# Kernel tuning notes

Measured on AMD Instinct MI355X. Metric: run time of the kernel, lower is better.

## Reference

```python
import jax, jax.numpy as jnp
import numpy as np

B, T, RNN_DIM, ENC_DIM, ATT_DIM, NFILT, KSIZE = 256, 1024, 1024, 512, 128, 32, 31
PAD = (KSIZE - 1) // 2


def setup_inputs() -> dict:
    key = jax.random.key(0)
    ks = jax.random.split(key, 10)
    attn = jax.random.uniform(ks[3], (B, T), dtype=jnp.float32)
    attn = attn / jnp.sum(attn, axis=1, keepdims=True)  # previous-step alignment (sums to 1)
    return {
        "query": jax.random.normal(ks[0], (B, RNN_DIM), dtype=jnp.float32),
        "memory": jax.random.normal(ks[1], (B, T, ENC_DIM), dtype=jnp.float32),
        "processed_memory": jax.random.normal(ks[2], (B, T, ATT_DIM), dtype=jnp.float32),
        "attn_weights": attn,
        "attn_weights_cum": jax.random.uniform(ks[4], (B, T), dtype=jnp.float32),
        "memory_lengths": jax.random.randint(ks[5], (B,), T // 2, T + 1),
        "conv_w": jax.random.normal(ks[6], (NFILT, 2, KSIZE), dtype=jnp.float32) * 0.1,
        "W_loc": jax.random.normal(ks[7], (ATT_DIM, NFILT), dtype=jnp.float32) * 0.1,
        "W_q": jax.random.normal(ks[8], (ATT_DIM, RNN_DIM), dtype=jnp.float32) * 0.03,
        "v_w": jax.random.normal(ks[9], (1, ATT_DIM), dtype=jnp.float32) * 0.1,
        "v_b": jnp.zeros((1,), dtype=jnp.float32),
    }


def reference(query, memory, processed_memory, attn_weights, attn_weights_cum,
              memory_lengths, conv_w, W_loc, W_q, v_w, v_b):
    Tlen = memory.shape[1]
    # [B, 2, T]: stack prev + cumulative alignments
    cat = jnp.stack([attn_weights, attn_weights_cum], axis=1)
    # location conv: Conv1d(2 -> NFILT, k=31, same padding, no bias) -> [B, NFILT, T]
    loc = jax.lax.conv_general_dilated(
        cat, conv_w, window_strides=(1,), padding=[(PAD, PAD)],
        dimension_numbers=("NCH", "OIH", "NCH"))
    # location_dense: [B, T, ATT_DIM]
    processed_location = jnp.einsum("bct,ac->bta", loc, W_loc)
    # query projection: [B, 1, ATT_DIM]
    processed_query = (query @ W_q.T)[:, None, :]
    # additive energies: v . tanh(q + loc + mem) -> [B, T]
    hidden = jnp.tanh(processed_query + processed_location + processed_memory)
    energies = jnp.einsum("bta,a->bt", hidden, v_w[0]) + v_b[0]
    # mask padded positions (pos >= length) with -inf
    mask = jnp.arange(Tlen)[None, :] >= memory_lengths[:, None]
    energies = jnp.where(mask, -jnp.inf, energies)
    new_attn = jax.nn.softmax(energies, axis=1)
    new_cum = attn_weights_cum + new_attn
    # context: [B, ENC_DIM]
    context = jnp.einsum("bt,bte->be", new_attn, memory)
    return context, new_attn, new_cum
```

## Files before the change

kernel.cpp:

```cpp
#include <hip/hip_runtime.h>
#include <math.h>

#define Bc 256
#define Tc 1024
#define RNN_DIMc 1024
#define ENC_DIMc 512
#define ATT_DIMc 128
#define NFILTc 32
#define KSIZEc 31
#define PADc 15

typedef float f4v __attribute__((ext_vector_type(4)));

__device__ __forceinline__ float fast_tanh(float x) {
    x = fminf(15.f, fmaxf(-15.f, x));
    float z = __expf(2.f * x);
    return (z - 1.f) / (z + 1.f);
}

__device__ __forceinline__ float wave_reduce_max(float x) {
#pragma unroll
    for (int off = 32; off > 0; off >>= 1) x = fmaxf(x, __shfl_xor(x, off, 64));
    return x;
}

__device__ __forceinline__ float wave_reduce_sum(float x) {
#pragma unroll
    for (int off = 32; off > 0; off >>= 1) x += __shfl_xor(x, off, 64);
    return x;
}

__global__ __launch_bounds__(1024) void lsa_fused(
    const float* __restrict__ query, const float* __restrict__ memory,
    const float* __restrict__ pm, const float* __restrict__ attn_w,
    const float* __restrict__ cum_w, const int* __restrict__ lens,
    const float* __restrict__ conv_w, const float* __restrict__ W_loc,
    const float* __restrict__ W_q, const float* __restrict__ v_w,
    const float* __restrict__ v_b, float* __restrict__ ctx,
    float* __restrict__ out_attn, float* __restrict__ out_cum) {
    const int b = blockIdx.x;
    const int tid = threadIdx.x;
    const int len = lens[b];

    __shared__ float s_q[RNN_DIMc];
    __shared__ float s_pq[ATT_DIMc];
    __shared__ float s_win0[Tc + 2 * PADc];
    __shared__ float s_win1[Tc + 2 * PADc];
    __shared__ float s_attn[Tc];
    __shared__ float s_redm[16];
    __shared__ float s_reds[16];
    __shared__ float s_ctx[16][ENC_DIMc];

    s_q[tid] = query[b * RNN_DIMc + tid];
    for (int i = tid; i < Tc + 2 * PADc; i += 1024) {
        int tt = i - PADc;
        bool ok = (tt >= 0) && (tt < Tc);
        s_win0[i] = ok ? attn_w[b * Tc + tt] : 0.f;
        s_win1[i] = ok ? cum_w[b * Tc + tt] : 0.f;
    }
    __syncthreads();

    {
        const int a = tid >> 3;
        const int c = tid & 7;
        const float* w = W_q + (size_t)a * RNN_DIMc;
        float acc = 0.f;
#pragma unroll 4
        for (int j = 0; j < 32; ++j) {
            const int r = c * 4 + j * 32;
            float4 wv = *(const float4*)(w + r);
            acc = fmaf(wv.x, s_q[r + 0], acc);
            acc = fmaf(wv.y, s_q[r + 1], acc);
            acc = fmaf(wv.z, s_q[r + 2], acc);
            acc = fmaf(wv.w, s_q[r + 3], acc);
        }
        acc += __shfl_xor(acc, 1, 64);
        acc += __shfl_xor(acc, 2, 64);
        acc += __shfl_xor(acc, 4, 64);
        if (c == 0) s_pq[a] = acc;
    }
    __syncthreads();

    const int t = tid;
    float e = -INFINITY;
    if (t < len) {
        float loc[NFILTc];
#pragma unroll
        for (int f = 0; f < NFILTc; ++f) loc[f] = 0.f;
        for (int k = 0; k < KSIZEc; ++k) {
            const float wa = s_win0[t + k];
            const float wc = s_win1[t + k];
#pragma unroll
            for (int f = 0; f < NFILTc; ++f) {
                loc[f] = fmaf(conv_w[f * (2 * KSIZEc) + k], wa, loc[f]);
                loc[f] = fmaf(conv_w[f * (2 * KSIZEc) + KSIZEc + k], wc, loc[f]);
            }
        }

        const float* pmrow = pm + ((size_t)(b * Tc + t)) * ATT_DIMc;
        float acc = 0.f;
#pragma unroll 2
        for (int a = 0; a < ATT_DIMc; a += 4) {
            const f4v pmv = __builtin_nontemporal_load((const f4v*)(pmrow + a));
            const float* wl = W_loc + a * NFILTc;
            float pl0 = 0.f, pl1 = 0.f, pl2 = 0.f, pl3 = 0.f;
#pragma unroll
            for (int f = 0; f < NFILTc; ++f) {
                float lf = loc[f];
                pl0 = fmaf(wl[f], lf, pl0);
                pl1 = fmaf(wl[NFILTc + f], lf, pl1);
                pl2 = fmaf(wl[2 * NFILTc + f], lf, pl2);
                pl3 = fmaf(wl[3 * NFILTc + f], lf, pl3);
            }
            acc = fmaf(v_w[a + 0], fast_tanh(s_pq[a + 0] + pl0 + pmv.x), acc);
            acc = fmaf(v_w[a + 1], fast_tanh(s_pq[a + 1] + pl1 + pmv.y), acc);
            acc = fmaf(v_w[a + 2], fast_tanh(s_pq[a + 2] + pl2 + pmv.z), acc);
            acc = fmaf(v_w[a + 3], fast_tanh(s_pq[a + 3] + pl3 + pmv.w), acc);
        }
        e = acc + v_b[0];
    }

    {
        float m = wave_reduce_max(e);
        if ((tid & 63) == 0) s_redm[tid >> 6] = m;
        __syncthreads();
        float bm = s_redm[0];
#pragma unroll
        for (int j = 1; j < 16; ++j) bm = fmaxf(bm, s_redm[j]);

        float p = __expf(e - bm);
        float s = wave_reduce_sum(p);
        if ((tid & 63) == 0) s_reds[tid >> 6] = s;
        __syncthreads();
        float tot = 0.f;
#pragma unroll
        for (int j = 0; j < 16; ++j) tot += s_reds[j];
        float na = p * (1.f / tot);

        out_attn[b * Tc + t] = na;
        out_cum[b * Tc + t] = s_win1[t + PADc] + na;
        s_attn[t] = na;
    }
    __syncthreads();

    {
        const int tr = tid >> 6;
        const int e8 = (tid & 63) * 8;
        const float* mb = memory + (size_t)b * Tc * ENC_DIMc;
        f4v acc0 = {0.f, 0.f, 0.f, 0.f};
        f4v acc1 = {0.f, 0.f, 0.f, 0.f};
#pragma unroll 4
        for (int tt = tr; tt < len; tt += 16) {
            const float w = s_attn[tt];
            const float* row = mb + (size_t)tt * ENC_DIMc + e8;
            const f4v m0 = __builtin_nontemporal_load((const f4v*)(row));
            const f4v m1 = __builtin_nontemporal_load((const f4v*)(row + 4));
            acc0.x = fmaf(w, m0.x, acc0.x);
            acc0.y = fmaf(w, m0.y, acc0.y);
            acc0.z = fmaf(w, m0.z, acc0.z);
            acc0.w = fmaf(w, m0.w, acc0.w);
            acc1.x = fmaf(w, m1.x, acc1.x);
            acc1.y = fmaf(w, m1.y, acc1.y);
            acc1.z = fmaf(w, m1.z, acc1.z);
            acc1.w = fmaf(w, m1.w, acc1.w);
        }
        *(f4v*)&s_ctx[tr][e8] = acc0;
        *(f4v*)&s_ctx[tr][e8 + 4] = acc1;
    }
    __syncthreads();
    if (tid < ENC_DIMc) {
        float s = 0.f;
#pragma unroll
        for (int j = 0; j < 16; ++j) s += s_ctx[j][tid];
        ctx[b * ENC_DIMc + tid] = s;
    }
}

extern "C" void kernel_launch(void* const* d_in, const int* in_sizes, int n_in,
                              void* d_out, int out_size, void* d_ws, size_t ws_size,
                              hipStream_t stream) {
    const float* query  = (const float*)d_in[0];
    const float* memory = (const float*)d_in[1];
    const float* pm     = (const float*)d_in[2];
    const float* attn_w = (const float*)d_in[3];
    const float* cum_w  = (const float*)d_in[4];
    const int*   lens   = (const int*)d_in[5];
    const float* conv_w = (const float*)d_in[6];
    const float* W_loc  = (const float*)d_in[7];
    const float* W_q    = (const float*)d_in[8];
    const float* v_w    = (const float*)d_in[9];
    const float* v_b    = (const float*)d_in[10];

    float* out      = (float*)d_out;
    float* ctx      = out;
    float* out_attn = out + Bc * ENC_DIMc;
    float* out_cum  = out + Bc * ENC_DIMc + Bc * Tc;


    lsa_fused<<<Bc, 1024, 0, stream>>>(query, memory, pm, attn_w, cum_w, lens,
                                       conv_w, W_loc, W_q, v_w, v_b,
                                       ctx, out_attn, out_cum);
}
```

Measured before the change: 799.3 us.

## Split context reduction into separate chunked kernels for more parallelism

The fused kernel becomes three launches. The first computes energies, softmax and the cumulative output. The second computes per-chunk partial context sums with 16 blocks per batch row. The third adds the partials into the final context. This spreads the memory read (the largest stream) over 4096 smaller blocks instead of 256 large ones, so HBM bandwidth use and occupancy should improve. The cost is two extra launches, writing and re-reading the attention weights and partials through global memory, and a workspace buffer.

```diff
diff --git a/kernel.cpp b/kernel.cpp
--- a/kernel.cpp
+++ b/kernel.cpp
@@ -9,6 +9,8 @@
 #define NFILTc 32
 #define KSIZEc 31
 #define PADc 15
+#define NCH 16
+#define CHT (Tc / NCH)
 
 typedef float f4v __attribute__((ext_vector_type(4)));
 
@@ -30,13 +32,12 @@
     return x;
 }
 
-__global__ __launch_bounds__(1024) void lsa_fused(
-    const float* __restrict__ query, const float* __restrict__ memory,
-    const float* __restrict__ pm, const float* __restrict__ attn_w,
-    const float* __restrict__ cum_w, const int* __restrict__ lens,
-    const float* __restrict__ conv_w, const float* __restrict__ W_loc,
-    const float* __restrict__ W_q, const float* __restrict__ v_w,
-    const float* __restrict__ v_b, float* __restrict__ ctx,
+__global__ __launch_bounds__(1024) void lsa_energy(
+    const float* __restrict__ query, const float* __restrict__ pm,
+    const float* __restrict__ attn_w, const float* __restrict__ cum_w,
+    const int* __restrict__ lens, const float* __restrict__ conv_w,
+    const float* __restrict__ W_loc, const float* __restrict__ W_q,
+    const float* __restrict__ v_w, const float* __restrict__ v_b,
     float* __restrict__ out_attn, float* __restrict__ out_cum) {
     const int b = blockIdx.x;
     const int tid = threadIdx.x;
@@ -46,10 +47,8 @@
     __shared__ float s_pq[ATT_DIMc];
     __shared__ float s_win0[Tc + 2 * PADc];
     __shared__ float s_win1[Tc + 2 * PADc];
-    __shared__ float s_attn[Tc];
     __shared__ float s_redm[16];
     __shared__ float s_reds[16];
-    __shared__ float s_ctx[16][ENC_DIMc];
 
     s_q[tid] = query[b * RNN_DIMc + tid];
     for (int i = tid; i < Tc + 2 * PADc; i += 1024) {
@@ -96,7 +95,6 @@
                 loc[f] = fmaf(conv_w[f * (2 * KSIZEc) + KSIZEc + k], wc, loc[f]);
             }
         }
-
         const float* pmrow = pm + ((size_t)(b * Tc + t)) * ATT_DIMc;
         float acc = 0.f;
 #pragma unroll 2
@@ -139,41 +137,66 @@
 
         out_attn[b * Tc + t] = na;
         out_cum[b * Tc + t] = s_win1[t + PADc] + na;
-        s_attn[t] = na;
-    }
-    __syncthreads();
-
-    {
-        const int tr = tid >> 6;
-        const int e8 = (tid & 63) * 8;
-        const float* mb = memory + (size_t)b * Tc * ENC_DIMc;
-        f4v acc0 = {0.f, 0.f, 0.f, 0.f};
-        f4v acc1 = {0.f, 0.f, 0.f, 0.f};
+    }
+}
+
+__global__ __launch_bounds__(256) void ctx_part_k(
+    const float* __restrict__ memory, const float* __restrict__ out_attn,
+    const int* __restrict__ lens, float* __restrict__ part) {
+    const int bc = blockIdx.x;
+    const int b = bc >> 4;
+    const int ch = bc & (NCH - 1);
+    const int t0 = ch * CHT;
+    const int tid = threadIdx.x;
+    const int len = lens[b];
+    if (t0 >= len) return;
+    int lim = len - t0;
+    if (lim > CHT) lim = CHT;
+
+    __shared__ float s_w[CHT];
+    __shared__ float s_part[4][ENC_DIMc];
+    if (tid < CHT) s_w[tid] = out_attn[b * Tc + t0 + tid];
+    __syncthreads();
+
+    const int tr = tid >> 6;
+    const int e8 = (tid & 63) * 8;
+    const float* mb = memory + ((size_t)(b * Tc + t0)) * ENC_DIMc;
+    f4v acc0 = {0.f, 0.f, 0.f, 0.f};
+    f4v acc1 = {0.f, 0.f, 0.f, 0.f};
 #pragma unroll 4
-        for (int tt = tr; tt < len; tt += 16) {
-            const float w = s_attn[tt];
-            const float* row = mb + (size_t)tt * ENC_DIMc + e8;
-            const f4v m0 = __builtin_nontemporal_load((const f4v*)(row));
-            const f4v m1 = __builtin_nontemporal_load((const f4v*)(row + 4));
-            acc0.x = fmaf(w, m0.x, acc0.x);
-            acc0.y = fmaf(w, m0.y, acc0.y);
-            acc0.z = fmaf(w, m0.z, acc0.z);
-            acc0.w = fmaf(w, m0.w, acc0.w);
-            acc1.x = fmaf(w, m1.x, acc1.x);
-            acc1.y = fmaf(w, m1.y, acc1.y);
-            acc1.z = fmaf(w, m1.z, acc1.z);
-            acc1.w = fmaf(w, m1.w, acc1.w);
-        }
-        *(f4v*)&s_ctx[tr][e8] = acc0;
-        *(f4v*)&s_ctx[tr][e8 + 4] = acc1;
-    }
-    __syncthreads();
-    if (tid < ENC_DIMc) {
-        float s = 0.f;
-#pragma unroll
-        for (int j = 0; j < 16; ++j) s += s_ctx[j][tid];
-        ctx[b * ENC_DIMc + tid] = s;
-    }
+    for (int tt = tr; tt < lim; tt += 4) {
+        const float w = s_w[tt];
+        const float* row = mb + (size_t)tt * ENC_DIMc + e8;
+        const f4v m0 = __builtin_nontemporal_load((const f4v*)(row));
+        const f4v m1 = __builtin_nontemporal_load((const f4v*)(row + 4));
+        acc0.x = fmaf(w, m0.x, acc0.x);
+        acc0.y = fmaf(w, m0.y, acc0.y);
+        acc0.z = fmaf(w, m0.z, acc0.z);
+        acc0.w = fmaf(w, m0.w, acc0.w);
+        acc1.x = fmaf(w, m1.x, acc1.x);
+        acc1.y = fmaf(w, m1.y, acc1.y);
+        acc1.z = fmaf(w, m1.z, acc1.z);
+        acc1.w = fmaf(w, m1.w, acc1.w);
+    }
+    *(f4v*)&s_part[tr][e8] = acc0;
+    *(f4v*)&s_part[tr][e8 + 4] = acc1;
+    __syncthreads();
+    for (int e2 = tid; e2 < ENC_DIMc; e2 += 256) {
+        float v = s_part[0][e2] + s_part[1][e2] + s_part[2][e2] + s_part[3][e2];
+        part[(size_t)bc * ENC_DIMc + e2] = v;
+    }
+}
+
+__global__ __launch_bounds__(512) void ctx_comb_k(
+    const float* __restrict__ part, const int* __restrict__ lens,
+    float* __restrict__ ctx) {
+    const int b = blockIdx.x;
+    const int tid = threadIdx.x;
+    const int nch = (lens[b] + CHT - 1) / CHT;
+    const float* p = part + (size_t)(b * NCH) * ENC_DIMc + tid;
+    float s = 0.f;
+    for (int ch = 0; ch < nch; ++ch) s += p[(size_t)ch * ENC_DIMc];
+    ctx[b * ENC_DIMc + tid] = s;
 }
 
 extern "C" void kernel_launch(void* const* d_in, const int* in_sizes, int n_in,
@@ -196,8 +219,11 @@
     float* out_attn = out + Bc * ENC_DIMc;
     float* out_cum  = out + Bc * ENC_DIMc + Bc * Tc;
 
-
-    lsa_fused<<<Bc, 1024, 0, stream>>>(query, memory, pm, attn_w, cum_w, lens,
-                                       conv_w, W_loc, W_q, v_w, v_b,
-                                       ctx, out_attn, out_cum);
-}
+    float* part = (float*)d_ws;
+
+    lsa_energy<<<Bc, 1024, 0, stream>>>(query, pm, attn_w, cum_w, lens,
+                                        conv_w, W_loc, W_q, v_w, v_b,
+                                        out_attn, out_cum);
+    ctx_part_k<<<Bc * NCH, 256, 0, stream>>>(memory, out_attn, lens, part);
+    ctx_comb_k<<<Bc, 512, 0, stream>>>(part, lens, ctx);
+}
```

After: 818.1 us. 1.02x slower.

## Convert fused attention kernel to persistent work queue with chunked context tasks

Applied to the files above, without the earlier changes.

Replaces the one-block-per-batch kernel with a persistent kernel of 1024 blocks of 256 threads. Blocks pull tasks from an atomic counter: first the per-batch energy and softmax tasks, then per-batch, per-time-chunk context partial sums. Context tasks wait on a release/acquire flag set when their batch's softmax finishes, and the last chunk to finish reduces the partials. The aim is to raise parallelism for the memory-bound context read over the 256 MB memory tensor, and to overlap it with energy work. This costs an extra init kernel, workspace traffic, spin-waiting and fewer threads per energy task.

```diff
diff --git a/kernel.cpp b/kernel.cpp
--- a/kernel.cpp
+++ b/kernel.cpp
@@ -9,6 +9,11 @@
 #define NFILTc 32
 #define KSIZEc 31
 #define PADc 15
+#define CHTc 128
+#define NCHc 8
+#define N_ENERGY Bc
+#define NTASKS (N_ENERGY + Bc * NCHc)
+#define FLAG_STRIDE 16
 
 typedef float f4v __attribute__((ext_vector_type(4)));
 
@@ -30,149 +35,212 @@
     return x;
 }
 
-__global__ __launch_bounds__(1024) void lsa_fused(
+__global__ __launch_bounds__(256) void init_k(int* __restrict__ ctrl) {
+    ctrl[blockIdx.x * 256 + threadIdx.x] = 0;
+}
+
+__global__ __launch_bounds__(256, 4) void lsa_persist(
     const float* __restrict__ query, const float* __restrict__ memory,
     const float* __restrict__ pm, const float* __restrict__ attn_w,
     const float* __restrict__ cum_w, const int* __restrict__ lens,
     const float* __restrict__ conv_w, const float* __restrict__ W_loc,
     const float* __restrict__ W_q, const float* __restrict__ v_w,
-    const float* __restrict__ v_b, float* __restrict__ ctx,
+    const float* __restrict__ v_b, int* __restrict__ ctrl,
+    float* __restrict__ part, float* __restrict__ ctx,
     float* __restrict__ out_attn, float* __restrict__ out_cum) {
-    const int b = blockIdx.x;
-    const int tid = threadIdx.x;
-    const int len = lens[b];
 
     __shared__ float s_q[RNN_DIMc];
     __shared__ float s_pq[ATT_DIMc];
+    __shared__ float s_pqh[ATT_DIMc];
     __shared__ float s_win0[Tc + 2 * PADc];
     __shared__ float s_win1[Tc + 2 * PADc];
-    __shared__ float s_attn[Tc];
-    __shared__ float s_redm[16];
-    __shared__ float s_reds[16];
-    __shared__ float s_ctx[16][ENC_DIMc];
-
-    s_q[tid] = query[b * RNN_DIMc + tid];
-    for (int i = tid; i < Tc + 2 * PADc; i += 1024) {
-        int tt = i - PADc;
-        bool ok = (tt >= 0) && (tt < Tc);
-        s_win0[i] = ok ? attn_w[b * Tc + tt] : 0.f;
-        s_win1[i] = ok ? cum_w[b * Tc + tt] : 0.f;
-    }
-    __syncthreads();
-
-    {
-        const int a = tid >> 3;
-        const int c = tid & 7;
-        const float* w = W_q + (size_t)a * RNN_DIMc;
-        float acc = 0.f;
+    __shared__ float s_e[Tc];
+    __shared__ float s_red[4];
+    __shared__ float s_red2[4];
+    __shared__ float s_w[CHTc];
+    __shared__ float s_part[4][ENC_DIMc];
+    __shared__ int s_task;
+    __shared__ int s_old;
+
+    const int tid = threadIdx.x;
+    int* flags   = ctrl;
+    int* done    = ctrl + Bc * FLAG_STRIDE;
+    int* counter = done + Bc;
+
+    while (true) {
+        __syncthreads();
+        if (tid == 0) s_task = atomicAdd(counter, 1);
+        __syncthreads();
+        const int task = s_task;
+        if (task >= NTASKS) return;
+
+        if (task < N_ENERGY) {
+            const int b = task;
+            const int len = lens[b];
+            {
+                const int i4 = tid * 4;
+                *(f4v*)&s_q[i4] = *(const f4v*)&query[(size_t)b * RNN_DIMc + i4];
+            }
+            for (int i = tid; i < Tc + 2 * PADc; i += 256) {
+                int tt = i - PADc;
+                bool ok = (tt >= 0) && (tt < Tc);
+                s_win0[i] = ok ? attn_w[b * Tc + tt] : 0.f;
+                s_win1[i] = ok ? cum_w[b * Tc + tt] : 0.f;
+            }
+            __syncthreads();
+            {
+                const int a = tid & 127;
+                const int h = tid >> 7;
+                const float* w = W_q + (size_t)a * RNN_DIMc + h * 512;
+                const float* qq = s_q + h * 512;
+                float acc = 0.f;
 #pragma unroll 4
-        for (int j = 0; j < 32; ++j) {
-            const int r = c * 4 + j * 32;
-            float4 wv = *(const float4*)(w + r);
-            acc = fmaf(wv.x, s_q[r + 0], acc);
-            acc = fmaf(wv.y, s_q[r + 1], acc);
-            acc = fmaf(wv.z, s_q[r + 2], acc);
-            acc = fmaf(wv.w, s_q[r + 3], acc);
+                for (int r = 0; r < 512; r += 4) {
+                    float4 wv = *(const float4*)(w + r);
+                    acc = fmaf(wv.x, qq[r + 0], acc);
+                    acc = fmaf(wv.y, qq[r + 1], acc);
+                    acc = fmaf(wv.z, qq[r + 2], acc);
+                    acc = fmaf(wv.w, qq[r + 3], acc);
+                }
+                if (h) s_pqh[a] = acc; else s_pq[a] = acc;
+            }
+            __syncthreads();
+            if (tid < ATT_DIMc) s_pq[tid] += s_pqh[tid];
+            __syncthreads();
+
+            for (int sct = 0; sct < 4; ++sct) {
+                const int t = (sct << 8) + tid;
+                float e = -INFINITY;
+                if (t < len) {
+                    float loc[NFILTc];
+#pragma unroll
+                    for (int f = 0; f < NFILTc; ++f) loc[f] = 0.f;
+                    for (int k = 0; k < KSIZEc; ++k) {
+                        const float wa = s_win0[t + k];
+                        const float wc = s_win1[t + k];
+#pragma unroll
+                        for (int f = 0; f < NFILTc; ++f) {
+                            loc[f] = fmaf(conv_w[f * (2 * KSIZEc) + k], wa, loc[f]);
+                            loc[f] = fmaf(conv_w[f * (2 * KSIZEc) + KSIZEc + k], wc, loc[f]);
+                        }
+                    }
+                    const float* pmrow = pm + ((size_t)(b * Tc + t)) * ATT_DIMc;
+                    float acc = 0.f;
+#pragma unroll 2
+                    for (int a = 0; a < ATT_DIMc; a += 4) {
+                        const f4v pmv = __builtin_nontemporal_load((const f4v*)(pmrow + a));
+                        const float* wl = W_loc + a * NFILTc;
+                        float pl0 = 0.f, pl1 = 0.f, pl2 = 0.f, pl3 = 0.f;
+#pragma unroll
+                        for (int f = 0; f < NFILTc; ++f) {
+                            float lf = loc[f];
+                            pl0 = fmaf(wl[f], lf, pl0);
+                            pl1 = fmaf(wl[NFILTc + f], lf, pl1);
+                            pl2 = fmaf(wl[2 * NFILTc + f], lf, pl2);
+                            pl3 = fmaf(wl[3 * NFILTc + f], lf, pl3);
+                        }
+                        acc = fmaf(v_w[a + 0], fast_tanh(s_pq[a + 0] + pl0 + pmv.x), acc);
+                        acc = fmaf(v_w[a + 1], fast_tanh(s_pq[a + 1] + pl1 + pmv.y), acc);
+                        acc = fmaf(v_w[a + 2], fast_tanh(s_pq[a + 2] + pl2 + pmv.z), acc);
+                        acc = fmaf(v_w[a + 3], fast_tanh(s_pq[a + 3] + pl3 + pmv.w), acc);
+                    }
+                    e = acc + v_b[0];
+                }
+                s_e[t] = e;
+            }
+            __syncthreads();
+            {
+                float m4 = fmaxf(fmaxf(s_e[tid], s_e[tid + 256]),
+                                 fmaxf(s_e[tid + 512], s_e[tid + 768]));
+                float m = wave_reduce_max(m4);
+                if ((tid & 63) == 0) s_red[tid >> 6] = m;
+                __syncthreads();
+                const float bm = fmaxf(fmaxf(s_red[0], s_red[1]), fmaxf(s_red[2], s_red[3]));
+                float psum = 0.f;
+#pragma unroll
+                for (int sct = 0; sct < 4; ++sct) {
+                    const int t = (sct << 8) + tid;
+                    float p = __expf(s_e[t] - bm);
+                    s_e[t] = p;
+                    psum += p;
+                }
+                float sw = wave_reduce_sum(psum);
+                if ((tid & 63) == 0) s_red2[tid >> 6] = sw;
+                __syncthreads();
+                const float inv = 1.f / (s_red2[0] + s_red2[1] + s_red2[2] + s_red2[3]);
+#pragma unroll
+                for (int sct = 0; sct < 4; ++sct) {
+                    const int t = (sct << 8) + tid;
+                    const float na = s_e[t] * inv;
+                    out_attn[b * Tc + t] = na;
+                    out_cum[b * Tc + t] = s_win1[t + PADc] + na;
+                }
+            }
+            __syncthreads();
+            if (tid == 0)
+                __hip_atomic_store(&flags[b * FLAG_STRIDE], 1,
+                                   __ATOMIC_RELEASE, __HIP_MEMORY_SCOPE_AGENT);
+        } else {
+            const int idx = task - N_ENERGY;
+            const int b = idx & (Bc - 1);
+            const int ch = idx >> 8;
+            const int t0 = ch * CHTc;
+            const int len = lens[b];
+            if (t0 < len) {
+                if (tid == 0) {
+                    while (__hip_atomic_load(&flags[b * FLAG_STRIDE],
+                                             __ATOMIC_ACQUIRE, __HIP_MEMORY_SCOPE_AGENT) == 0)
+                        __builtin_amdgcn_s_sleep(8);
+                }
+                __syncthreads();
+                int lim = len - t0;
+                if (lim > CHTc) lim = CHTc;
+                if (tid < CHTc) s_w[tid] = out_attn[b * Tc + t0 + tid];
+                __syncthreads();
+
+                const int tr = tid >> 6;
+                const int e8 = (tid & 63) * 8;
+                const float* mb = memory + ((size_t)(b * Tc + t0)) * ENC_DIMc;
+                f4v acc0 = {0.f, 0.f, 0.f, 0.f};
+                f4v acc1 = {0.f, 0.f, 0.f, 0.f};
+#pragma unroll 4
+                for (int tt = tr; tt < lim; tt += 4) {
+                    const float wgt = s_w[tt];
+                    const float* row = mb + (size_t)tt * ENC_DIMc + e8;
+                    const f4v m0 = __builtin_nontemporal_load((const f4v*)(row));
+                    const f4v m1 = __builtin_nontemporal_load((const f4v*)(row + 4));
+                    acc0.x = fmaf(wgt, m0.x, acc0.x);
+                    acc0.y = fmaf(wgt, m0.y, acc0.y);
+                    acc0.z = fmaf(wgt, m0.z, acc0.z);
+                    acc0.w = fmaf(wgt, m0.w, acc0.w);
+                    acc1.x = fmaf(wgt, m1.x, acc1.x);
+                    acc1.y = fmaf(wgt, m1.y, acc1.y);
+                    acc1.z = fmaf(wgt, m1.z, acc1.z);
+                    acc1.w = fmaf(wgt, m1.w, acc1.w);
+                }
+                *(f4v*)&s_part[tr][e8] = acc0;
+                *(f4v*)&s_part[tr][e8 + 4] = acc1;
+                __syncthreads();
+                const size_t pbase = (size_t)(b * NCHc + ch) * ENC_DIMc;
+                for (int c = tid; c < ENC_DIMc; c += 256)
+                    part[pbase + c] = s_part[0][c] + s_part[1][c] + s_part[2][c] + s_part[3][c];
+                __syncthreads();
+                if (tid == 0)
+                    s_old = __hip_atomic_fetch_add(&done[b], 1,
+                                                   __ATOMIC_ACQ_REL, __HIP_MEMORY_SCOPE_AGENT);
+                __syncthreads();
+                const int nact = (len + CHTc - 1) >> 7;
+                if (s_old == nact - 1) {
+                    const float* pb = part + (size_t)b * NCHc * ENC_DIMc;
+                    for (int c = tid; c < ENC_DIMc; c += 256) {
+                        float sfin = 0.f;
+                        for (int c2 = 0; c2 < nact; ++c2)
+                            sfin += pb[(size_t)c2 * ENC_DIMc + c];
+                        ctx[b * ENC_DIMc + c] = sfin;
+                    }
+                }
+            }
         }
-        acc += __shfl_xor(acc, 1, 64);
-        acc += __shfl_xor(acc, 2, 64);
-        acc += __shfl_xor(acc, 4, 64);
-        if (c == 0) s_pq[a] = acc;
-    }
-    __syncthreads();
-
-    const int t = tid;
-    float e = -INFINITY;
-    if (t < len) {
-        float loc[NFILTc];
-#pragma unroll
-        for (int f = 0; f < NFILTc; ++f) loc[f] = 0.f;
-        for (int k = 0; k < KSIZEc; ++k) {
-            const float wa = s_win0[t + k];
-            const float wc = s_win1[t + k];
-#pragma unroll
-            for (int f = 0; f < NFILTc; ++f) {
-                loc[f] = fmaf(conv_w[f * (2 * KSIZEc) + k], wa, loc[f]);
-                loc[f] = fmaf(conv_w[f * (2 * KSIZEc) + KSIZEc + k], wc, loc[f]);
-            }
-        }
-
-        const float* pmrow = pm + ((size_t)(b * Tc + t)) * ATT_DIMc;
-        float acc = 0.f;
-#pragma unroll 2
-        for (int a = 0; a < ATT_DIMc; a += 4) {
-            const f4v pmv = __builtin_nontemporal_load((const f4v*)(pmrow + a));
-            const float* wl = W_loc + a * NFILTc;
-            float pl0 = 0.f, pl1 = 0.f, pl2 = 0.f, pl3 = 0.f;
-#pragma unroll
-            for (int f = 0; f < NFILTc; ++f) {
-                float lf = loc[f];
-                pl0 = fmaf(wl[f], lf, pl0);
-                pl1 = fmaf(wl[NFILTc + f], lf, pl1);
-                pl2 = fmaf(wl[2 * NFILTc + f], lf, pl2);
-                pl3 = fmaf(wl[3 * NFILTc + f], lf, pl3);
-            }
-            acc = fmaf(v_w[a + 0], fast_tanh(s_pq[a + 0] + pl0 + pmv.x), acc);
-            acc = fmaf(v_w[a + 1], fast_tanh(s_pq[a + 1] + pl1 + pmv.y), acc);
-            acc = fmaf(v_w[a + 2], fast_tanh(s_pq[a + 2] + pl2 + pmv.z), acc);
-            acc = fmaf(v_w[a + 3], fast_tanh(s_pq[a + 3] + pl3 + pmv.w), acc);
-        }
-        e = acc + v_b[0];
-    }
-
-    {
-        float m = wave_reduce_max(e);
-        if ((tid & 63) == 0) s_redm[tid >> 6] = m;
-        __syncthreads();
-        float bm = s_redm[0];
-#pragma unroll
-        for (int j = 1; j < 16; ++j) bm = fmaxf(bm, s_redm[j]);
-
-        float p = __expf(e - bm);
-        float s = wave_reduce_sum(p);
-        if ((tid & 63) == 0) s_reds[tid >> 6] = s;
-        __syncthreads();
-        float tot = 0.f;
-#pragma unroll
-        for (int j = 0; j < 16; ++j) tot += s_reds[j];
-        float na = p * (1.f / tot);
-
-        out_attn[b * Tc + t] = na;
-        out_cum[b * Tc + t] = s_win1[t + PADc] + na;
-        s_attn[t] = na;
-    }
-    __syncthreads();
-
-    {
-        const int tr = tid >> 6;
-        const int e8 = (tid & 63) * 8;
-        const float* mb = memory + (size_t)b * Tc * ENC_DIMc;
-        f4v acc0 = {0.f, 0.f, 0.f, 0.f};
-        f4v acc1 = {0.f, 0.f, 0.f, 0.f};
-#pragma unroll 4
-        for (int tt = tr; tt < len; tt += 16) {
-            const float w = s_attn[tt];
-            const float* row = mb + (size_t)tt * ENC_DIMc + e8;
-            const f4v m0 = __builtin_nontemporal_load((const f4v*)(row));
-            const f4v m1 = __builtin_nontemporal_load((const f4v*)(row + 4));
-            acc0.x = fmaf(w, m0.x, acc0.x);
-            acc0.y = fmaf(w, m0.y, acc0.y);
-            acc0.z = fmaf(w, m0.z, acc0.z);
-            acc0.w = fmaf(w, m0.w, acc0.w);
-            acc1.x = fmaf(w, m1.x, acc1.x);
-            acc1.y = fmaf(w, m1.y, acc1.y);
-            acc1.z = fmaf(w, m1.z, acc1.z);
-            acc1.w = fmaf(w, m1.w, acc1.w);
-        }
-        *(f4v*)&s_ctx[tr][e8] = acc0;
-        *(f4v*)&s_ctx[tr][e8 + 4] = acc1;
-    }
-    __syncthreads();
-    if (tid < ENC_DIMc) {
-        float s = 0.f;
-#pragma unroll
-        for (int j = 0; j < 16; ++j) s += s_ctx[j][tid];
-        ctx[b * ENC_DIMc + tid] = s;
     }
 }
 
@@ -196,8 +264,11 @@
     float* out_attn = out + Bc * ENC_DIMc;
     float* out_cum  = out + Bc * ENC_DIMc + Bc * Tc;
 
-
-    lsa_fused<<<Bc, 1024, 0, stream>>>(query, memory, pm, attn_w, cum_w, lens,
-                                       conv_w, W_loc, W_q, v_w, v_b,
-                                       ctx, out_attn, out_cum);
-}
+    int*   ctrl = (int*)d_ws;
+    float* part = (float*)d_ws + 8192;
+
+    init_k<<<18, 256, 0, stream>>>(ctrl);
+    lsa_persist<<<1024, 256, 0, stream>>>(query, memory, pm, attn_w, cum_w, lens,
+                                          conv_w, W_loc, W_q, v_w, v_b,
+                                          ctrl, part, ctx, out_attn, out_cum);
+}
```

After: 1.612 ms. +101.7%, slower.
